# Performance work log

Measured on AMD Instinct MI355X. Metric: run time of the kernel, lower is better.

Reference implementation:

```python
import jax, jax.numpy as jnp
import numpy as np

B, T, H, NH, V = 2, 2048, 512, 8, 32000
HD = H // NH  # head dim

def setup_inputs() -> dict:
    key = jax.random.key(0)
    ks = jax.random.split(key, 15)
    s = 0.02
    rn = lambda k, shp: (jax.random.normal(k, shp, dtype=jnp.float32) * s)
    return {
        "ixs": jax.random.randint(ks[0], (B, T), 0, V, dtype=jnp.int32),
        "tok_emb": rn(ks[1], (V, H)),
        "pos_emb": rn(ks[2], (1, T, H)),
        "W_prj": rn(ks[3], (H, H)),
        "Wq": rn(ks[4], (H, H)), "bq": rn(ks[5], (H,)),
        "Wk": rn(ks[6], (H, H)), "bk": rn(ks[7], (H,)),
        "Wv": rn(ks[8], (H, H)), "bv": rn(ks[9], (H,)),
        "W1": rn(ks[10], (H, H)), "b1": rn(ks[11], (H,)),
        "W2": rn(ks[12], (V, H)), "b2": rn(ks[13], (V,)),
    }

def reference(ixs, tok_emb, pos_emb, W_prj, Wq, bq, Wk, bk, Wv, bv, W1, b1, W2, b2):
    b, t = ixs.shape
    # embeddings + projection (prj1 has no bias)
    x = tok_emb[ixs] + pos_emb[:, :t, :]          # [B,T,H]
    x = x @ W_prj.T                                # [B,T,H]
    # multi-head causal attention; NOTE: scale uses full hidden dim (allH**0.5)
    def heads(W, bias):
        return (x @ W.T + bias).reshape(b, t, NH, HD).transpose(0, 2, 1, 3)  # [B,nH,T,HD]
    q, k, v = heads(Wq, bq), heads(Wk, bk), heads(Wv, bv)
    att = jnp.einsum('bhqd,bhkd->bhqk', q, k) / (H ** 0.5)  # [B,nH,T,T]
    causal = jnp.tril(jnp.ones((t, t), dtype=bool))
    att = jnp.where(causal, att, -jnp.inf)
    w = jax.nn.softmax(att, axis=-1)
    y = jnp.einsum('bhqk,bhkd->bhqd', w, v)        # [B,nH,T,HD]
    y = y.transpose(0, 2, 1, 3).reshape(b, t, H)   # [B,T,H]
    # MLP: Linear->ReLU->Linear->ReLU (final ReLU per original loop condition)
    h1 = jax.nn.relu(y @ W1.T + b1)                # [B,T,H]
    out = jax.nn.relu(h1 @ W2.T + b2)              # [B,T,V]
    return out
```

## Files before the change

kernel.cpp:

```cpp
#include <hip/hip_runtime.h>
#include <stdint.h>
#include <stddef.h>

#define TSEQ   2048
#define HDIM   512
#define NHEADS 8
#define HEADD  64
#define NVOCAB 32000
#define NROWS  4096

typedef unsigned short ushort_t;
typedef __bf16 bf16x8 __attribute__((ext_vector_type(8)));
typedef float  f32x4  __attribute__((ext_vector_type(4)));
typedef unsigned short us8 __attribute__((ext_vector_type(8)));
typedef unsigned short us4 __attribute__((ext_vector_type(4)));
typedef unsigned short us2 __attribute__((ext_vector_type(2)));

__device__ __forceinline__ ushort_t f2bf(float f){
  union { float f; unsigned int u; } v; v.f = f;
  unsigned int u = v.u;
  u += 0x7FFFu + ((u >> 16) & 1u);
  return (ushort_t)(u >> 16);
}

__device__ __forceinline__ void gload_lds16(const ushort_t* g, ushort_t* l){
  __builtin_amdgcn_global_load_lds(
      (const __attribute__((address_space(1))) void*)g,
      (__attribute__((address_space(3))) void*)l, 16, 0, 0);
}

#define CVT_N4   4423680
#define CVT_TOT  4424064
__global__ void cvt_all_kernel(const float* __restrict__ Wprj, const float* __restrict__ Wq,
                               const float* __restrict__ Wk,   const float* __restrict__ Wv,
                               const float* __restrict__ W1,   const float* __restrict__ W2,
                               const float* __restrict__ bq,   const float* __restrict__ bk,
                               const float* __restrict__ bv,
                               ushort_t* __restrict__ wdst, float* __restrict__ bqkv){
  int stride = gridDim.x * blockDim.x;
  for (int i = blockIdx.x * blockDim.x + threadIdx.x; i < CVT_TOT; i += stride){
    if (i < CVT_N4){
      const float* src; int j;
      if (i < 327680){
        int w = i >> 16;
        j = i & 65535;
        src = (w == 0) ? Wprj : (w == 1) ? Wq : (w == 2) ? Wk : (w == 3) ? Wv : W1;
      } else {
        j = i - 327680;
        src = W2;
      }
      float4 f = ((const float4*)src)[j];
      us4 o;
      o[0] = f2bf(f.x); o[1] = f2bf(f.y); o[2] = f2bf(f.z); o[3] = f2bf(f.w);
      ((us4*)wdst)[i] = o;
    } else {
      int j = i - CVT_N4;
      const float* src = (j < 128) ? bq : (j < 256) ? bk : bv;
      int jj = j & 127;
      ((float4*)bqkv)[j] = ((const float4*)src)[jj];
    }
  }
}

__global__ void embed_kernel(const int* __restrict__ ixs, const float* __restrict__ tok,
                             const float* __restrict__ pos, ushort_t* __restrict__ x0){
  const int r = blockIdx.x;
  const int t = r & (TSEQ - 1);
  const int ix = ixs[r];
  const int j = threadIdx.x;
  const float2 a = ((const float2*)(tok + (size_t)ix * HDIM))[j];
  const float2 p = ((const float2*)(pos + (size_t)t * HDIM))[j];
  us2 o; o[0] = f2bf(a.x + p.x); o[1] = f2bf(a.y + p.y);
  *(us2*)(x0 + (size_t)r * HDIM + j * 2) = o;
}

template<int HAS_BIAS, int RELU, int OUT_F32>
__global__ __launch_bounds__(256) void gemm_bt_kernel(
    const ushort_t* __restrict__ A, const ushort_t* __restrict__ W,
    const float* __restrict__ bias, void* __restrict__ outp,
    int M, int N, int K)
{
  __shared__ ushort_t As[128 * 64];
  __shared__ ushort_t Bs[128 * 64];
  const int tid  = threadIdx.x;
  const int wave = tid >> 6;
  const int lane = tid & 63;
  const int lr   = lane & 15;
  const int lg   = lane >> 4;
  const int nby  = M >> 7;
  const int by   = blockIdx.x % nby;
  const int bx   = blockIdx.x / nby;
  const int row0 = by << 7;
  const int col0 = bx << 7;
  const int wr   = wave >> 1, wc = wave & 1;

  f32x4 acc[4][4];
#pragma unroll
  for (int m = 0; m < 4; m++)
#pragma unroll
    for (int n = 0; n < 4; n++) acc[m][n] = (f32x4){0.f, 0.f, 0.f, 0.f};

  const int e    = tid * 8;
  const int srow = e >> 6;
  const int scol = e & 63;
  const ushort_t* gA = A + (size_t)(row0 + srow) * K + scol;
  const ushort_t* gB = W + (size_t)(col0 + srow) * K + scol;
  const int ldsbase = wave * 512;

  for (int kt = 0; kt < K; kt += 64){
#pragma unroll
    for (int p = 0; p < 4; p++){
      gload_lds16(gA + (size_t)(p * 32) * K + kt, &As[p * 2048 + ldsbase]);
      gload_lds16(gB + (size_t)(p * 32) * K + kt, &Bs[p * 2048 + ldsbase]);
    }
    __syncthreads();
#pragma unroll
    for (int kk = 0; kk < 64; kk += 32){
      bf16x8 af[4], bfr[4];
#pragma unroll
      for (int m = 0; m < 4; m++)
        af[m] = __builtin_bit_cast(bf16x8,
            *(const us8*)&As[(wr * 64 + m * 16 + lr) * 64 + kk + lg * 8]);
#pragma unroll
      for (int n = 0; n < 4; n++)
        bfr[n] = __builtin_bit_cast(bf16x8,
            *(const us8*)&Bs[(wc * 64 + n * 16 + lr) * 64 + kk + lg * 8]);
#pragma unroll
      for (int m = 0; m < 4; m++)
#pragma unroll
        for (int n = 0; n < 4; n++)
          acc[m][n] = __builtin_amdgcn_mfma_f32_16x16x32_bf16(af[m], bfr[n], acc[m][n], 0, 0, 0);
    }
    __syncthreads();
  }

#pragma unroll
  for (int n = 0; n < 4; n++){
    const int col = col0 + wc * 64 + n * 16 + lr;
    float bv = 0.f;
    if (HAS_BIAS) bv = bias[col];
#pragma unroll
    for (int m = 0; m < 4; m++){
      const int rowb = row0 + wr * 64 + m * 16 + lg * 4;
#pragma unroll
      for (int r = 0; r < 4; r++){
        float vv = acc[m][n][r] + bv;
        if (RELU) vv = fmaxf(vv, 0.f);
        const size_t o = (size_t)(rowb + r) * N + col;
        if (OUT_F32) ((float*)outp)[o] = vv;
        else         ((ushort_t*)outp)[o] = f2bf(vv);
      }
    }
  }
}

#define NKT 16
__global__ __launch_bounds__(512, 2) void gemm_big_kernel(
    const ushort_t* __restrict__ A, const ushort_t* __restrict__ W,
    const float* __restrict__ bias, float* __restrict__ outp,
    int M, int N, int K)
{
  __shared__ ushort_t Asb[3][256 * 32];
  __shared__ ushort_t Bsb[3][256 * 32];
  const int tid  = threadIdx.x;
  const int wave = tid >> 6;
  const int lane = tid & 63;
  const int lr   = lane & 15;
  const int lg   = lane >> 4;
  const int wr   = wave >> 2;
  const int wc   = wave & 3;
  const int nby  = M >> 8;
  const int by   = blockIdx.x % nby;
  const int bx   = blockIdx.x / nby;
  const int row0 = by << 8;
  const int col0 = bx << 8;

  const int rA   = tid >> 2;
  const int csw  = ((tid & 3) ^ (rA & 3) ^ ((rA >> 2) & 3)) * 8;
  const int swzc = (lg ^ (lr & 3) ^ ((lr >> 2) & 3)) * 8;

  f32x4 acc[8][4];
#pragma unroll
  for (int m = 0; m < 8; m++)
#pragma unroll
    for (int n = 0; n < 4; n++) acc[m][n] = (f32x4){0.f, 0.f, 0.f, 0.f};

  {
    const ushort_t* gA = A + (size_t)(row0 + rA) * K + csw;
    const ushort_t* gW = W + (size_t)(col0 + rA) * K + csw;
#pragma unroll
    for (int t = 0; t < 2; t++){
      gload_lds16(gA + t * 32,                       &Asb[t][wave * 512]);
      gload_lds16(gA + (size_t)128 * K + t * 32,     &Asb[t][4096 + wave * 512]);
      gload_lds16(gW + t * 32,                       &Bsb[t][wave * 512]);
      gload_lds16(gW + (size_t)128 * K + t * 32,     &Bsb[t][4096 + wave * 512]);
    }
  }
  asm volatile("s_waitcnt vmcnt(4)" ::: "memory");
  __builtin_amdgcn_s_barrier();

  for (int t = 0; t < NKT; ++t){
    const ushort_t* Ac = &Asb[t % 3][0];
    const ushort_t* Bc = &Bsb[t % 3][0];
    ushort_t* An = &Asb[(t + 2) % 3][0];
    ushort_t* Bn = &Bsb[(t + 2) % 3][0];
    const bool pf = (t + 2 < NKT);
    const int kg = (t + 2) * 32;

    bf16x8 bfr[4], af[4];
#pragma unroll
    for (int n = 0; n < 4; n++)
      bfr[n] = __builtin_bit_cast(bf16x8,
          *(const us8*)&Bc[(wc * 64 + n * 16 + lr) * 32 + swzc]);
#pragma unroll
    for (int q = 0; q < 4; q++)
      af[q] = __builtin_bit_cast(bf16x8,
          *(const us8*)&Ac[(wr * 128 + q * 16 + lr) * 32 + swzc]);
    if (pf){
      gload_lds16(A + (size_t)(row0 + rA) * K + kg + csw,       An + wave * 512);
      gload_lds16(A + (size_t)(row0 + rA + 128) * K + kg + csw, An + 4096 + wave * 512);
    }
    __builtin_amdgcn_s_barrier();
    asm volatile("s_waitcnt lgkmcnt(0)" ::: "memory");
    __builtin_amdgcn_sched_barrier(0);
    __builtin_amdgcn_s_setprio(1);
#pragma unroll
    for (int q = 0; q < 4; q++)
#pragma unroll
      for (int n = 0; n < 4; n++)
        acc[q][n] = __builtin_amdgcn_mfma_f32_16x16x32_bf16(af[q], bfr[n], acc[q][n], 0, 0, 0);
    __builtin_amdgcn_s_setprio(0);
    __builtin_amdgcn_sched_barrier(0);
    __builtin_amdgcn_s_barrier();

#pragma unroll
    for (int q = 0; q < 4; q++)
      af[q] = __builtin_bit_cast(bf16x8,
          *(const us8*)&Ac[(wr * 128 + (q + 4) * 16 + lr) * 32 + swzc]);
    if (pf){
      gload_lds16(W + (size_t)(col0 + rA) * K + kg + csw,       Bn + wave * 512);
      gload_lds16(W + (size_t)(col0 + rA + 128) * K + kg + csw, Bn + 4096 + wave * 512);
    }
    __builtin_amdgcn_s_barrier();
    asm volatile("s_waitcnt lgkmcnt(0)" ::: "memory");
    __builtin_amdgcn_sched_barrier(0);
    __builtin_amdgcn_s_setprio(1);
#pragma unroll
    for (int q = 0; q < 4; q++)
#pragma unroll
      for (int n = 0; n < 4; n++)
        acc[q + 4][n] = __builtin_amdgcn_mfma_f32_16x16x32_bf16(af[q], bfr[n], acc[q + 4][n], 0, 0, 0);
    __builtin_amdgcn_s_setprio(0);
    __builtin_amdgcn_sched_barrier(0);
    if (t < NKT - 2) { asm volatile("s_waitcnt vmcnt(4)" ::: "memory"); }
    else             { asm volatile("s_waitcnt vmcnt(0)" ::: "memory"); }
    __builtin_amdgcn_s_barrier();
  }

  float bvv[4];
#pragma unroll
  for (int n = 0; n < 4; n++) bvv[n] = bias[col0 + wc * 64 + n * 16 + lr];
#pragma unroll
  for (int m = 0; m < 8; m++)
#pragma unroll
    for (int n = 0; n < 4; n++){
      const size_t o0 = (size_t)(row0 + wr * 128 + m * 16 + lg * 4) * N
                      + (col0 + wc * 64 + n * 16 + lr);
#pragma unroll
      for (int r = 0; r < 4; r++)
        outp[o0 + (size_t)r * N] = fmaxf(acc[m][n][r] + bvv[n], 0.f);
    }
}

__global__ __launch_bounds__(256) void attn_kernel(
    const ushort_t* __restrict__ qkv, ushort_t* __restrict__ y)
{
  __shared__ ushort_t Ks[64 * 64];
  __shared__ ushort_t Vt[64 * 64];
  __shared__ ushort_t Ps[4][16 * 64];
  const int qt   = 31 - blockIdx.x;
  const int hb   = blockIdx.y;
  const int b    = hb >> 3;
  const int h    = hb & 7;
  const int tid  = threadIdx.x;
  const int wave = tid >> 6, lane = tid & 63;
  const int lr   = lane & 15, lg = lane >> 4;
  const int ld   = 3 * HDIM;
  const size_t rowbase = (size_t)b * TSEQ;
  const ushort_t* kb = qkv + HDIM;
  const ushort_t* vb = qkv + 2 * HDIM;

  const int qrow = qt * 64 + wave * 16 + lr;
  const ushort_t* qp = qkv + (rowbase + qrow) * ld + h * HEADD;
  bf16x8 qf[2];
  qf[0] = __builtin_bit_cast(bf16x8, *(const us8*)&qp[lg * 8]);
  qf[1] = __builtin_bit_cast(bf16x8, *(const us8*)&qp[32 + lg * 8]);

  float m_run[4], l_run[4];
  f32x4 acc_o[4];
#pragma unroll
  for (int i = 0; i < 4; i++){ m_run[i] = -1e30f; l_run[i] = 0.f; acc_o[i] = (f32x4){0,0,0,0}; }

  const int e    = tid * 8;
  const int srow = e >> 6;
  const int scol = e & 63;
  const float scale = 0.04419417382415922f;

  for (int kt = 0; kt <= qt; ++kt){
    const ushort_t* gK = kb + (rowbase + kt * 64 + srow) * ld + h * HEADD + scol;
    gload_lds16(gK,                     &Ks[wave * 512]);
    gload_lds16(gK + (size_t)32 * ld,   &Ks[2048 + wave * 512]);
    const ushort_t* gV = vb + (rowbase + kt * 64 + srow) * ld + h * HEADD + scol;
    us8 v0 = *(const us8*)gV;
    us8 v1 = *(const us8*)(gV + (size_t)32 * ld);
#pragma unroll
    for (int j = 0; j < 8; j++){
      Vt[(scol + j) * 64 + srow]      = v0[j];
      Vt[(scol + j) * 64 + srow + 32] = v1[j];
    }
    __syncthreads();

    f32x4 s[4];
#pragma unroll
    for (int n = 0; n < 4; n++){
      s[n] = (f32x4){0, 0, 0, 0};
#pragma unroll
      for (int ks = 0; ks < 2; ks++){
        bf16x8 kf = __builtin_bit_cast(bf16x8,
            *(const us8*)&Ks[(n * 16 + lr) * 64 + ks * 32 + lg * 8]);
        s[n] = __builtin_amdgcn_mfma_f32_16x16x32_bf16(qf[ks], kf, s[n], 0, 0, 0);
      }
    }

    float sv[4][4];
    float tmax[4] = {-1e30f, -1e30f, -1e30f, -1e30f};
    const bool diag = (kt == qt);
#pragma unroll
    for (int n = 0; n < 4; n++)
#pragma unroll
      for (int r = 0; r < 4; r++){
        float x = s[n][r] * scale;
        if (diag && (n * 16 + lr) > (wave * 16 + lg * 4 + r)) x = -1e30f;
        sv[n][r] = x;
        tmax[r] = fmaxf(tmax[r], x);
      }
#pragma unroll
    for (int off = 1; off < 16; off <<= 1)
#pragma unroll
      for (int r = 0; r < 4; r++) tmax[r] = fmaxf(tmax[r], __shfl_xor(tmax[r], off));

    float alpha[4], psum[4];
#pragma unroll
    for (int r = 0; r < 4; r++){
      float mn = fmaxf(m_run[r], tmax[r]);
      alpha[r] = __expf(m_run[r] - mn);
      m_run[r] = mn;
      psum[r] = 0.f;
    }
    float p[4][4];
#pragma unroll
    for (int n = 0; n < 4; n++)
#pragma unroll
      for (int r = 0; r < 4; r++){ p[n][r] = __expf(sv[n][r] - m_run[r]); psum[r] += p[n][r]; }
#pragma unroll
    for (int off = 1; off < 16; off <<= 1)
#pragma unroll
      for (int r = 0; r < 4; r++) psum[r] += __shfl_xor(psum[r], off);
#pragma unroll
    for (int r = 0; r < 4; r++) l_run[r] = l_run[r] * alpha[r] + psum[r];
#pragma unroll
    for (int nd = 0; nd < 4; nd++)
#pragma unroll
      for (int r = 0; r < 4; r++) acc_o[nd][r] *= alpha[r];

#pragma unroll
    for (int n = 0; n < 4; n++)
#pragma unroll
      for (int r = 0; r < 4; r++)
        Ps[wave][(lg * 4 + r) * 64 + n * 16 + lr] = f2bf(p[n][r]);
    asm volatile("s_waitcnt lgkmcnt(0)" ::: "memory");
    bf16x8 pa[2];
    pa[0] = __builtin_bit_cast(bf16x8, *(const us8*)&Ps[wave][lr * 64 + lg * 8]);
    pa[1] = __builtin_bit_cast(bf16x8, *(const us8*)&Ps[wave][lr * 64 + 32 + lg * 8]);
#pragma unroll
    for (int nd = 0; nd < 4; nd++)
#pragma unroll
      for (int ks = 0; ks < 2; ks++){
        bf16x8 vf = __builtin_bit_cast(bf16x8,
            *(const us8*)&Vt[(nd * 16 + lr) * 64 + ks * 32 + lg * 8]);
        acc_o[nd] = __builtin_amdgcn_mfma_f32_16x16x32_bf16(pa[ks], vf, acc_o[nd], 0, 0, 0);
      }
    __syncthreads();
  }

  float inv[4];
#pragma unroll
  for (int r = 0; r < 4; r++) inv[r] = 1.f / l_run[r];
#pragma unroll
  for (int nd = 0; nd < 4; nd++)
#pragma unroll
    for (int r = 0; r < 4; r++){
      const int row_t = qt * 64 + wave * 16 + lg * 4 + r;
      y[(rowbase + row_t) * HDIM + h * HEADD + nd * 16 + lr] = f2bf(acc_o[nd][r] * inv[r]);
    }
}

extern "C" void kernel_launch(void* const* d_in, const int* in_sizes, int n_in,
                              void* d_out, int out_size, void* d_ws, size_t ws_size,
                              hipStream_t stream)
{
  const int*   ixs  = (const int*)  d_in[0];
  const float* tok  = (const float*)d_in[1];
  const float* pos  = (const float*)d_in[2];
  const float* Wprj = (const float*)d_in[3];
  const float* Wq   = (const float*)d_in[4];
  const float* bq_  = (const float*)d_in[5];
  const float* Wk   = (const float*)d_in[6];
  const float* bk_  = (const float*)d_in[7];
  const float* Wv   = (const float*)d_in[8];
  const float* bv_  = (const float*)d_in[9];
  const float* W1   = (const float*)d_in[10];
  const float* b1_  = (const float*)d_in[11];
  const float* W2   = (const float*)d_in[12];
  const float* b2_  = (const float*)d_in[13];
  float* out = (float*)d_out;

  ushort_t* ws    = (ushort_t*)d_ws;
  ushort_t* x0    = ws;
  ushort_t* x1    = x0    + 2097152;
  ushort_t* qkv   = x1    + 2097152;
  ushort_t* yb    = qkv   + 6291456;
  ushort_t* h1b   = yb    + 2097152;
  ushort_t* wprjb = h1b   + 2097152;
  ushort_t* wqkvb = wprjb + 262144;
  ushort_t* w1b   = wqkvb + 786432;
  ushort_t* w2b   = w1b   + 262144;
  float*    bqkv  = (float*)(w2b + 16384000);

  cvt_all_kernel<<<2048, 256, 0, stream>>>(Wprj, Wq, Wk, Wv, W1, W2,
                                           bq_, bk_, bv_, wprjb, bqkv);

  embed_kernel<<<NROWS, 256, 0, stream>>>(ixs, tok, pos, x0);

  gemm_bt_kernel<0,0,0><<<32 * 4,   256, 0, stream>>>(x0,  wprjb, nullptr, x1,  NROWS, 512,   512);
  gemm_bt_kernel<1,0,0><<<32 * 12,  256, 0, stream>>>(x1,  wqkvb, bqkv,    qkv, NROWS, 1536,  512);
  attn_kernel<<<dim3(32, 16), 256, 0, stream>>>(qkv, yb);
  gemm_bt_kernel<1,1,0><<<32 * 4,   256, 0, stream>>>(yb,  w1b,   b1_,     h1b, NROWS, 512,   512);
  gemm_big_kernel<<<16 * 125, 512, 0, stream>>>(h1b, w2b, b2_, out, NROWS, NVOCAB, 512);
}
```

Baseline: 400.1 us.

## Double-buffer and swizzle small GEMMs, remap blocks across XCDs, vectorize epilogue stores

The small GEMM kernel now double-buffers its LDS tiles so the next k-tile loads while the current one computes. It also XOR-swizzles LDS columns to avoid bank conflicts and spreads workgroups across the 8 XCDs. Both GEMMs swap the MFMA operand order so each lane holds 4 consecutive output columns. The epilogues can then write 16-byte vector stores, with nontemporal stores for the large fp32 logits. The large GEMM hardcodes K and N and uses an XCD-aware block index mapping to improve L2 reuse. The cost is more LDS use in the small GEMM and hardcoded shapes in the big one.

```diff
diff --git a/kernel.cpp b/kernel.cpp
--- a/kernel.cpp
+++ b/kernel.cpp
@@ -75,24 +75,28 @@
 }
 
 template<int HAS_BIAS, int RELU, int OUT_F32>
-__global__ __launch_bounds__(256) void gemm_bt_kernel(
+__global__ __launch_bounds__(256) void gemm2_kernel(
     const ushort_t* __restrict__ A, const ushort_t* __restrict__ W,
     const float* __restrict__ bias, void* __restrict__ outp,
     int M, int N, int K)
 {
-  __shared__ ushort_t As[128 * 64];
-  __shared__ ushort_t Bs[128 * 64];
+  __shared__ ushort_t As[2][128 * 64];
+  __shared__ ushort_t Bs[2][128 * 64];
   const int tid  = threadIdx.x;
   const int wave = tid >> 6;
   const int lane = tid & 63;
   const int lr   = lane & 15;
   const int lg   = lane >> 4;
-  const int nby  = M >> 7;
-  const int by   = blockIdx.x % nby;
-  const int bx   = blockIdx.x / nby;
+  const int wr   = wave >> 1, wc = wave & 1;
+
+  const int nwg = gridDim.x;
+  const int cpx = nwg >> 3;
+  const int g   = (blockIdx.x & 7) * cpx + (blockIdx.x >> 3);
+  const int nby = M >> 7;
+  const int by  = g % nby;
+  const int bx  = g / nby;
   const int row0 = by << 7;
   const int col0 = bx << 7;
-  const int wr   = wave >> 1, wc = wave & 1;
 
   f32x4 acc[4][4];
 #pragma unroll
@@ -102,53 +106,67 @@
 
   const int e    = tid * 8;
   const int srow = e >> 6;
-  const int scol = e & 63;
-  const ushort_t* gA = A + (size_t)(row0 + srow) * K + scol;
-  const ushort_t* gB = W + (size_t)(col0 + srow) * K + scol;
-  const int ldsbase = wave * 512;
-
-  for (int kt = 0; kt < K; kt += 64){
-#pragma unroll
-    for (int p = 0; p < 4; p++){
-      gload_lds16(gA + (size_t)(p * 32) * K + kt, &As[p * 2048 + ldsbase]);
-      gload_lds16(gB + (size_t)(p * 32) * K + kt, &Bs[p * 2048 + ldsbase]);
-    }
-    __syncthreads();
+  const int gch  = (((e & 63) >> 3) ^ (srow & 7)) * 8;
+  const ushort_t* gA = A + (size_t)(row0 + srow) * K + gch;
+  const ushort_t* gB = W + (size_t)(col0 + srow) * K + gch;
+  const int ldsoff = wave * 512;
+
+#pragma unroll
+  for (int p = 0; p < 4; p++){
+    gload_lds16(gA + (size_t)(p * 32) * K, &As[0][p * 2048 + ldsoff]);
+    gload_lds16(gB + (size_t)(p * 32) * K, &Bs[0][p * 2048 + ldsoff]);
+  }
+  __syncthreads();
+
+  const int NT = K >> 6;
+  for (int t = 0; t < NT; ++t){
+    const int cur = t & 1;
+    if (t + 1 < NT){
+      const int ko = (t + 1) << 6;
+#pragma unroll
+      for (int p = 0; p < 4; p++){
+        gload_lds16(gA + (size_t)(p * 32) * K + ko, &As[cur ^ 1][p * 2048 + ldsoff]);
+        gload_lds16(gB + (size_t)(p * 32) * K + ko, &Bs[cur ^ 1][p * 2048 + ldsoff]);
+      }
+    }
 #pragma unroll
     for (int kk = 0; kk < 64; kk += 32){
+      const int rch = (((kk >> 3) + lg) ^ (lr & 7)) * 8;
       bf16x8 af[4], bfr[4];
 #pragma unroll
       for (int m = 0; m < 4; m++)
         af[m] = __builtin_bit_cast(bf16x8,
-            *(const us8*)&As[(wr * 64 + m * 16 + lr) * 64 + kk + lg * 8]);
+            *(const us8*)&As[cur][(wr * 64 + m * 16 + lr) * 64 + rch]);
 #pragma unroll
       for (int n = 0; n < 4; n++)
         bfr[n] = __builtin_bit_cast(bf16x8,
-            *(const us8*)&Bs[(wc * 64 + n * 16 + lr) * 64 + kk + lg * 8]);
+            *(const us8*)&Bs[cur][(wc * 64 + n * 16 + lr) * 64 + rch]);
 #pragma unroll
       for (int m = 0; m < 4; m++)
 #pragma unroll
         for (int n = 0; n < 4; n++)
-          acc[m][n] = __builtin_amdgcn_mfma_f32_16x16x32_bf16(af[m], bfr[n], acc[m][n], 0, 0, 0);
+          acc[m][n] = __builtin_amdgcn_mfma_f32_16x16x32_bf16(bfr[n], af[m], acc[m][n], 0, 0, 0);
     }
     __syncthreads();
   }
 
 #pragma unroll
   for (int n = 0; n < 4; n++){
-    const int col = col0 + wc * 64 + n * 16 + lr;
-    float bv = 0.f;
-    if (HAS_BIAS) bv = bias[col];
+    const int colb = col0 + wc * 64 + n * 16 + lg * 4;
+    f32x4 b4 = (f32x4){0.f, 0.f, 0.f, 0.f};
+    if (HAS_BIAS) b4 = *(const f32x4*)&bias[colb];
 #pragma unroll
     for (int m = 0; m < 4; m++){
-      const int rowb = row0 + wr * 64 + m * 16 + lg * 4;
-#pragma unroll
-      for (int r = 0; r < 4; r++){
-        float vv = acc[m][n][r] + bv;
-        if (RELU) vv = fmaxf(vv, 0.f);
-        const size_t o = (size_t)(rowb + r) * N + col;
-        if (OUT_F32) ((float*)outp)[o] = vv;
-        else         ((ushort_t*)outp)[o] = f2bf(vv);
+      const int row = row0 + wr * 64 + m * 16 + lr;
+      float v0 = acc[m][n][0] + b4[0], v1 = acc[m][n][1] + b4[1];
+      float v2 = acc[m][n][2] + b4[2], v3 = acc[m][n][3] + b4[3];
+      if (RELU){ v0 = fmaxf(v0,0.f); v1 = fmaxf(v1,0.f); v2 = fmaxf(v2,0.f); v3 = fmaxf(v3,0.f); }
+      if (OUT_F32){
+        f32x4 o = {v0, v1, v2, v3};
+        *(f32x4*)&((float*)outp)[(size_t)row * N + colb] = o;
+      } else {
+        us4 o; o[0] = f2bf(v0); o[1] = f2bf(v1); o[2] = f2bf(v2); o[3] = f2bf(v3);
+        *(us4*)&((ushort_t*)outp)[(size_t)row * N + colb] = o;
       }
     }
   }
@@ -157,11 +175,11 @@
 #define NKT 16
 __global__ __launch_bounds__(512, 2) void gemm_big_kernel(
     const ushort_t* __restrict__ A, const ushort_t* __restrict__ W,
-    const float* __restrict__ bias, float* __restrict__ outp,
-    int M, int N, int K)
+    const float* __restrict__ bias, float* __restrict__ outp)
 {
   __shared__ ushort_t Asb[3][256 * 32];
   __shared__ ushort_t Bsb[3][256 * 32];
+  const int K = HDIM, N = NVOCAB;
   const int tid  = threadIdx.x;
   const int wave = tid >> 6;
   const int lane = tid & 63;
@@ -169,9 +187,9 @@
   const int lg   = lane >> 4;
   const int wr   = wave >> 2;
   const int wc   = wave & 3;
-  const int nby  = M >> 8;
-  const int by   = blockIdx.x % nby;
-  const int bx   = blockIdx.x / nby;
+  const int tt   = (blockIdx.x & 7) * 250 + (blockIdx.x >> 3);
+  const int bx   = tt >> 4;
+  const int by   = tt & 15;
   const int row0 = by << 8;
   const int col0 = bx << 8;
 
@@ -228,7 +246,7 @@
     for (int q = 0; q < 4; q++)
 #pragma unroll
       for (int n = 0; n < 4; n++)
-        acc[q][n] = __builtin_amdgcn_mfma_f32_16x16x32_bf16(af[q], bfr[n], acc[q][n], 0, 0, 0);
+        acc[q][n] = __builtin_amdgcn_mfma_f32_16x16x32_bf16(bfr[n], af[q], acc[q][n], 0, 0, 0);
     __builtin_amdgcn_s_setprio(0);
     __builtin_amdgcn_sched_barrier(0);
     __builtin_amdgcn_s_barrier();
@@ -249,7 +267,7 @@
     for (int q = 0; q < 4; q++)
 #pragma unroll
       for (int n = 0; n < 4; n++)
-        acc[q + 4][n] = __builtin_amdgcn_mfma_f32_16x16x32_bf16(af[q], bfr[n], acc[q + 4][n], 0, 0, 0);
+        acc[q + 4][n] = __builtin_amdgcn_mfma_f32_16x16x32_bf16(bfr[n], af[q], acc[q + 4][n], 0, 0, 0);
     __builtin_amdgcn_s_setprio(0);
     __builtin_amdgcn_sched_barrier(0);
     if (t < NKT - 2) { asm volatile("s_waitcnt vmcnt(4)" ::: "memory"); }
@@ -257,19 +275,21 @@
     __builtin_amdgcn_s_barrier();
   }
 
-  float bvv[4];
-#pragma unroll
-  for (int n = 0; n < 4; n++) bvv[n] = bias[col0 + wc * 64 + n * 16 + lr];
-#pragma unroll
-  for (int m = 0; m < 8; m++)
-#pragma unroll
-    for (int n = 0; n < 4; n++){
-      const size_t o0 = (size_t)(row0 + wr * 128 + m * 16 + lg * 4) * N
-                      + (col0 + wc * 64 + n * 16 + lr);
-#pragma unroll
-      for (int r = 0; r < 4; r++)
-        outp[o0 + (size_t)r * N] = fmaxf(acc[m][n][r] + bvv[n], 0.f);
-    }
+#pragma unroll
+  for (int n = 0; n < 4; n++){
+    const int colb = col0 + wc * 64 + n * 16 + lg * 4;
+    const f32x4 b4 = *(const f32x4*)&bias[colb];
+#pragma unroll
+    for (int m = 0; m < 8; m++){
+      const int row = row0 + wr * 128 + m * 16 + lr;
+      f32x4 o;
+      o[0] = fmaxf(acc[m][n][0] + b4[0], 0.f);
+      o[1] = fmaxf(acc[m][n][1] + b4[1], 0.f);
+      o[2] = fmaxf(acc[m][n][2] + b4[2], 0.f);
+      o[3] = fmaxf(acc[m][n][3] + b4[3], 0.f);
+      __builtin_nontemporal_store(o, (f32x4*)&outp[(size_t)row * N + colb]);
+    }
+  }
 }
 
 __global__ __launch_bounds__(256) void attn_kernel(
@@ -442,9 +462,9 @@
 
   embed_kernel<<<NROWS, 256, 0, stream>>>(ixs, tok, pos, x0);
 
-  gemm_bt_kernel<0,0,0><<<32 * 4,   256, 0, stream>>>(x0,  wprjb, nullptr, x1,  NROWS, 512,   512);
-  gemm_bt_kernel<1,0,0><<<32 * 12,  256, 0, stream>>>(x1,  wqkvb, bqkv,    qkv, NROWS, 1536,  512);
+  gemm2_kernel<0,0,0><<<32 * 4,   256, 0, stream>>>(x0,  wprjb, nullptr, x1,  NROWS, 512,   512);
+  gemm2_kernel<1,0,0><<<32 * 12,  256, 0, stream>>>(x1,  wqkvb, bqkv,    qkv, NROWS, 1536,  512);
   attn_kernel<<<dim3(32, 16), 256, 0, stream>>>(qkv, yb);
-  gemm_bt_kernel<1,1,0><<<32 * 4,   256, 0, stream>>>(yb,  w1b,   b1_,     h1b, NROWS, 512,   512);
-  gemm_big_kernel<<<16 * 125, 512, 0, stream>>>(h1b, w2b, b2_, out, NROWS, NVOCAB, 512);
-}
+  gemm2_kernel<1,1,0><<<32 * 4,   256, 0, stream>>>(yb,  w1b,   b1_,     h1b, NROWS, 512,   512);
+  gemm_big_kernel<<<2000, 512, 0, stream>>>(h1b, w2b, b2_, out);
+}
```

Result: slower. 421.5 us (+5.3%).
